# Optimization experiments

Measured on AMD Instinct MI355X. Metric: run time of the kernel, lower is better.

Reference implementation:

```python
import jax, jax.numpy as jnp
import numpy as np

N_NODES = 100000

def _gcn_layer(x, W, b, src, dst, n):
    # x: [N, Fin], W: [Fin, Fout], b: [Fout]; edges src->dst, [E]
    h = x @ W  # [N, Fout]
    # add self loops
    loops = jnp.arange(n, dtype=src.dtype)
    s = jnp.concatenate([src, loops])
    d = jnp.concatenate([dst, loops])
    # symmetric GCN normalization: deg^{-1/2}[s] * deg^{-1/2}[d]
    deg = jax.ops.segment_sum(jnp.ones_like(d, dtype=h.dtype), d, num_segments=n)
    dis = jnp.where(deg > 0, jax.lax.rsqrt(jnp.maximum(deg, 1.0)), 0.0)
    norm = dis[s] * dis[d]  # [E+N]
    msg = h[s] * norm[:, None]  # [E+N, Fout]
    out = jax.ops.segment_sum(msg, d, num_segments=n)  # [N, Fout]
    return out + b


def setup_inputs() -> dict:
    key = jax.random.key(0)
    k1, k2, k3, k4, k5 = jax.random.split(key, 5)
    in_feat, hidden, out_feat = 64, 128, 64
    n_edges = 1600000
    node_features = jax.random.normal(k1, (N_NODES, in_feat), dtype=jnp.float32)
    edge_index = jax.random.randint(k2, (2, n_edges), 0, N_NODES, dtype=jnp.int32)
    # glorot-ish params
    W1 = jax.random.normal(k3, (in_feat, hidden), dtype=jnp.float32) * (1.0 / np.sqrt(in_feat))
    b1 = jnp.zeros((hidden,), dtype=jnp.float32)
    W2 = jax.random.normal(k4, (hidden, out_feat), dtype=jnp.float32) * (1.0 / np.sqrt(hidden))
    b2 = jnp.zeros((out_feat,), dtype=jnp.float32)
    return {"node_features": node_features, "edge_index": edge_index,
            "W1": W1, "b1": b1, "W2": W2, "b2": b2}


def reference(node_features, edge_index, W1, b1, W2, b2):
    src, dst = edge_index[0], edge_index[1]
    n = node_features.shape[0]
    h = _gcn_layer(node_features, W1, b1, src, dst, n)
    h = jax.nn.relu(h)
    h = _gcn_layer(h, W2, b2, src, dst, n)
    return h
```

## Files before the change

kernel.cpp:

```cpp
#include <hip/hip_runtime.h>
#include <hip/hip_fp16.h>

#define NN 100000
#define NB 391
#define NG 512
#define REGION 6144

using f16x8 = __attribute__((ext_vector_type(8))) _Float16;
using f32x4 = __attribute__((ext_vector_type(4))) float;

__global__ __launch_bounds__(256) void bhist_kernel(const int* __restrict__ dst,
                                                    int* __restrict__ counts, int E) {
    __shared__ int h[NB];
    for (int i = threadIdx.x; i < NB; i += 256) h[i] = 0;
    __syncthreads();
    const int g = blockIdx.x;
    const int chunk = (E + NG - 1) / NG;
    const int lo = g * chunk, hi = min(E, lo + chunk);
    for (int e = lo + threadIdx.x; e < hi; e += 256) atomicAdd(&h[dst[e] >> 8], 1);
    __syncthreads();
    for (int i = threadIdx.x; i < NB; i += 256) counts[g * NB + i] = h[i];
}

__global__ __launch_bounds__(256) void bprefix_kernel(int* __restrict__ counts,
                                                      int* __restrict__ btot,
                                                      const float* __restrict__ W1,
                                                      const float* __restrict__ W2,
                                                      __half* __restrict__ W1t,
                                                      __half* __restrict__ W2t) {
    const int b = blockIdx.x, t = threadIdx.x;
    if (b == NB) {
        for (int i = t; i < 64 * 128; i += 256) {
            int k = i / 128, c = i % 128;
            W1t[c * 64 + k] = __float2half(W1[i]);
            int k2 = i / 64, c2 = i % 64;
            W2t[c2 * 128 + k2] = __float2half(W2[i]);
        }
        return;
    }
    __shared__ int sm[256];
    int loc[NG / 256];
    int s = 0;
    #pragma unroll
    for (int p = 0; p < NG / 256; ++p) {
        loc[p] = counts[((NG / 256) * t + p) * NB + b];
        s += loc[p];
    }
    sm[t] = s; __syncthreads();
    for (int off = 1; off < 256; off <<= 1) {
        int x = (t >= off) ? sm[t - off] : 0; __syncthreads();
        sm[t] += x; __syncthreads();
    }
    int run = b * REGION + sm[t] - s;
    #pragma unroll
    for (int p = 0; p < NG / 256; ++p) {
        int c = loc[p];
        counts[((NG / 256) * t + p) * NB + b] = run;
        run += c;
    }
    if (t == 255) btot[b] = sm[255];
}

__global__ __launch_bounds__(256) void bscatter_kernel(const int* __restrict__ src,
                                                       const int* __restrict__ dst,
                                                       const int* __restrict__ cstart,
                                                       int* __restrict__ staging, int E) {
    __shared__ int cur[NB];
    const int g = blockIdx.x;
    for (int i = threadIdx.x; i < NB; i += 256) cur[i] = cstart[g * NB + i];
    __syncthreads();
    const int chunk = (E + NG - 1) / NG;
    const int lo = g * chunk, hi = min(E, lo + chunk);
    for (int e = lo + threadIdx.x; e < hi; e += 256) {
        int d = dst[e];
        int pos = atomicAdd(&cur[d >> 8], 1);
        staging[pos] = src[e] | ((d & 255) << 17);
    }
}

__global__ __launch_bounds__(256) void bfinal_kernel(const int* __restrict__ btot,
                                                     const int* __restrict__ staging,
                                                     int* __restrict__ csr,
                                                     int* __restrict__ row_beg,
                                                     int* __restrict__ row_end,
                                                     float* __restrict__ dis,
                                                     const float* __restrict__ x,
                                                     __half* __restrict__ xh,
                                                     int N) {
    __shared__ int h[256];
    __shared__ int sc[256];
    __shared__ int cur[256];
    __shared__ float sdis[256];
    const int b = blockIdx.x, t = threadIdx.x;
    const int base = b * REGION;
    const int endb = base + btot[b];
    h[t] = 0; __syncthreads();
    for (int i = base + t; i < endb; i += 256) atomicAdd(&h[staging[i] >> 17], 1);
    __syncthreads();
    int v = h[t];
    sc[t] = v; __syncthreads();
    for (int off = 1; off < 256; off <<= 1) {
        int xv = (t >= off) ? sc[t - off] : 0; __syncthreads();
        sc[t] += xv; __syncthreads();
    }
    int excl = sc[t] - v;
    cur[t] = base + excl;
    float dv = rsqrtf((float)v + 1.0f);
    sdis[t] = dv;
    int node = b * 256 + t;
    if (node < N) {
        row_beg[node] = base + excl;
        row_end[node] = base + excl + v;
        dis[node] = dv;
    }
    __syncthreads();
    for (int i = base + t; i < endb; i += 256) {
        int p = staging[i];
        int pos = atomicAdd(&cur[p >> 17], 1);
        csr[pos] = p & 0x1FFFF;
    }
    const int node0 = b * 256;
    const int nmax = min(256, N - node0);
    for (int i = t; i < nmax * 16; i += 256) {
        int nl = i >> 4, c4 = i & 15;
        float4 vx = ((const float4*)x)[(size_t)(node0 + nl) * 16 + c4];
        float wq = sdis[nl];
        __half2* o = (__half2*)&xh[(size_t)(node0 + nl) * 64 + c4 * 4];
        o[0] = __floats2half2_rn(vx.x * wq, vx.y * wq);
        o[1] = __floats2half2_rn(vx.z * wq, vx.w * wq);
    }
}

__global__ __launch_bounds__(512) void gfuse_kernel(const __half* __restrict__ tab,
                                                    const float* __restrict__ dis,
                                                    const __half* __restrict__ W1t,
                                                    const float* __restrict__ b1,
                                                    const __half* __restrict__ W2t,
                                                    const int* __restrict__ row_beg,
                                                    const int* __restrict__ row_end,
                                                    const int* __restrict__ csr,
                                                    __half* __restrict__ zh, int N,
                                                    float one) {
    __shared__ _Float16 sA[16][72];
    __shared__ _Float16 sH[16][136];
    __shared__ float sP[4][16][16];
    const int tid = threadIdx.x;
    const int nodeL = tid >> 5;
    const int l32 = tid & 31;
    const int e = l32 >> 3;
    const int sub = l32 & 7;
    const int node0 = blockIdx.x * 16;
    const int node = node0 + nodeL;
    const int beg = row_beg[node], end = row_end[node];

    float acc[8];
    {
        f16x8 sv = *reinterpret_cast<const f16x8*>(&tab[(size_t)node * 64 + sub * 8]);
        #pragma unroll
        for (int q = 0; q < 8; ++q) acc[q] = (e == 0) ? (float)sv[q] : 0.0f;
    }
    for (int j = beg + e; j < end; j += 4) {
        int s = csr[j];
        f16x8 v = *reinterpret_cast<const f16x8*>(&tab[(size_t)s * 64 + sub * 8]);
        #pragma unroll
        for (int q = 0; q < 8; ++q) acc[q] = fmaf((float)v[q], one, acc[q]);
    }
    #pragma unroll
    for (int q = 0; q < 8; ++q) {
        acc[q] += __shfl_xor(acc[q], 8);
        acc[q] += __shfl_xor(acc[q], 16);
    }
    if (e == 0) {
        const float dd = dis[node];
        f16x8 o;
        #pragma unroll
        for (int q = 0; q < 8; ++q) o[q] = (_Float16)(acc[q] * dd);
        *reinterpret_cast<f16x8*>(&sA[nodeL][sub * 8]) = o;
    }
    __syncthreads();

    const int w = tid >> 6, lane = tid & 63;
    const int lrow = lane & 15, kgrp = lane >> 4;
    {
        const int col = w * 16 + lrow;
        f32x4 a1 = (f32x4){0.f, 0.f, 0.f, 0.f};
        #pragma unroll
        for (int ks = 0; ks < 2; ++ks) {
            const int kbase = ks * 32 + kgrp * 8;
            f16x8 a  = *reinterpret_cast<const f16x8*>(&sA[lrow][kbase]);
            f16x8 bf = *reinterpret_cast<const f16x8*>(&W1t[(size_t)col * 64 + kbase]);
            a1 = __builtin_amdgcn_mfma_f32_16x16x32_f16(a, bf, a1, 0, 0, 0);
        }
        const float bb = b1[col];
        #pragma unroll
        for (int r = 0; r < 4; ++r) {
            const int row = kgrp * 4 + r;
            sH[row][col] = (_Float16)fmaxf(a1[r] + bb, 0.0f);
        }
    }
    __syncthreads();
    {
        const int t2 = w & 3, kh = w >> 2;
        const int col = t2 * 16 + lrow;
        f32x4 a2 = (f32x4){0.f, 0.f, 0.f, 0.f};
        #pragma unroll
        for (int ks = 0; ks < 2; ++ks) {
            const int kbase = kh * 64 + ks * 32 + kgrp * 8;
            f16x8 a  = *reinterpret_cast<const f16x8*>(&sH[lrow][kbase]);
            f16x8 bf = *reinterpret_cast<const f16x8*>(&W2t[(size_t)col * 128 + kbase]);
            a2 = __builtin_amdgcn_mfma_f32_16x16x32_f16(a, bf, a2, 0, 0, 0);
        }
        if (kh == 1) {
            #pragma unroll
            for (int r = 0; r < 4; ++r) sP[t2][kgrp * 4 + r][lrow] = a2[r];
        }
        __syncthreads();
        if (kh == 0) {
            #pragma unroll
            for (int r = 0; r < 4; ++r) {
                const int row = kgrp * 4 + r;
                float v = (a2[r] + sP[t2][row][lrow]) * dis[node0 + row];
                zh[(size_t)(node0 + row) * 64 + col] = __float2half(v);
            }
        }
    }
}

__global__ __launch_bounds__(256) void gather2_kernel(const __half* __restrict__ tab,
                                                      const float* __restrict__ dis,
                                                      const float* __restrict__ b,
                                                      const int* __restrict__ row_beg,
                                                      const int* __restrict__ row_end,
                                                      const int* __restrict__ csr,
                                                      float* __restrict__ out, int N,
                                                      float one) {
    const int node = blockIdx.x * 4 + (threadIdx.x >> 6);
    const int lane = threadIdx.x & 63;
    const int g   = lane >> 3;
    const int sub = lane & 7;
    if (node >= N) return;
    const int beg = row_beg[node], end = row_end[node];

    float acc[8];
    {
        f16x8 sv = *reinterpret_cast<const f16x8*>(&tab[(size_t)node * 64 + sub * 8]);
        #pragma unroll
        for (int q = 0; q < 8; ++q) acc[q] = (g == 0) ? (float)sv[q] : 0.0f;
    }
    int j = beg;
    for (; j + 16 <= end; j += 16) {
        int sA = csr[j + g];
        int sB = csr[j + 8 + g];
        f16x8 vA = *reinterpret_cast<const f16x8*>(&tab[(size_t)sA * 64 + sub * 8]);
        f16x8 vB = *reinterpret_cast<const f16x8*>(&tab[(size_t)sB * 64 + sub * 8]);
        #pragma unroll
        for (int q = 0; q < 8; ++q) acc[q] = fmaf((float)vA[q], one, acc[q]);
        #pragma unroll
        for (int q = 0; q < 8; ++q) acc[q] = fmaf((float)vB[q], one, acc[q]);
    }
    if (j + 8 <= end) {
        int s = csr[j + g];
        f16x8 v = *reinterpret_cast<const f16x8*>(&tab[(size_t)s * 64 + sub * 8]);
        #pragma unroll
        for (int q = 0; q < 8; ++q) acc[q] = fmaf((float)v[q], one, acc[q]);
        j += 8;
    }
    if (j + g < end) {
        int s = csr[j + g];
        f16x8 v = *reinterpret_cast<const f16x8*>(&tab[(size_t)s * 64 + sub * 8]);
        #pragma unroll
        for (int q = 0; q < 8; ++q) acc[q] = fmaf((float)v[q], one, acc[q]);
    }
    #pragma unroll
    for (int q = 0; q < 8; ++q) {
        acc[q] += __shfl_xor(acc[q], 8);
        acc[q] += __shfl_xor(acc[q], 16);
        acc[q] += __shfl_xor(acc[q], 32);
    }
    if (g == 0) {
        const float dd = dis[node];
        float vv[8];
        #pragma unroll
        for (int q = 0; q < 8; ++q) vv[q] = acc[q] * dd + b[sub * 8 + q];
        float* op = &out[(size_t)node * 64 + sub * 8];
        *reinterpret_cast<float4*>(op)     = make_float4(vv[0], vv[1], vv[2], vv[3]);
        *reinterpret_cast<float4*>(op + 4) = make_float4(vv[4], vv[5], vv[6], vv[7]);
    }
}

extern "C" void kernel_launch(void* const* d_in, const int* in_sizes, int n_in,
                              void* d_out, int out_size, void* d_ws, size_t ws_size,
                              hipStream_t stream) {
    const float* x  = (const float*)d_in[0];
    const int*   ei = (const int*)d_in[1];
    const float* W1 = (const float*)d_in[2];
    const float* b1 = (const float*)d_in[3];
    const float* W2 = (const float*)d_in[4];
    const float* b2 = (const float*)d_in[5];
    float* out = (float*)d_out;

    const int N = NN;
    const int E = in_sizes[1] / 2;
    const int* src = ei;
    const int* dst = ei + E;

    int* counts   = (int*)d_ws;
    int* btot     = counts + NG * NB;
    int* row_beg  = btot + 512;
    int* row_end  = row_beg + N;
    float* dis    = (float*)(row_end + N);
    int* staging  = (int*)(dis + N);
    int* csr      = staging + (size_t)NB * REGION;
    float* base   = (float*)(csr + (size_t)NB * REGION);
    __half* xh    = (__half*)base;
    __half* zh    = (__half*)(base + (size_t)N * 32);
    __half* W1t   = (__half*)(base + (size_t)N * 64);
    __half* W2t   = W1t + 128 * 64;

    bhist_kernel<<<NG, 256, 0, stream>>>(dst, counts, E);
    bprefix_kernel<<<NB + 1, 256, 0, stream>>>(counts, btot, W1, W2, W1t, W2t);
    bscatter_kernel<<<NG, 256, 0, stream>>>(src, dst, counts, staging, E);
    bfinal_kernel<<<NB, 256, 0, stream>>>(btot, staging, csr, row_beg, row_end, dis, x, xh, N);

    gfuse_kernel<<<N / 16, 512, 0, stream>>>(xh, dis, W1t, b1, W2t, row_beg, row_end, csr, zh, N, 1.0f);

    gather2_kernel<<<N / 4, 256, 0, stream>>>(zh, dis, b2, row_beg, row_end, csr, out, N, 1.0f);
}
```

Baseline: 166.3 us.

## Split fused gather+GEMM kernel into separate gather and GEMM kernels

Layer-1 aggregation moves out of the fused gather+MFMA kernel into a standalone gather kernel. That kernel uses a full wave per node with 16-wide unrolling and writes an fp16 intermediate, and a separate GEMM kernel then reads it. The aim is to give the gather better occupancy and memory-level parallelism than the 512-thread fused block, where only 4 lanes per feature slice walked each edge list. In exchange it adds an extra kernel launch and a write and read of a 100k×64 fp16 intermediate.

```diff
diff --git a/kernel.cpp b/kernel.cpp
--- a/kernel.cpp
+++ b/kernel.cpp
@@ -131,36 +131,48 @@
     }
 }
 
-__global__ __launch_bounds__(512) void gfuse_kernel(const __half* __restrict__ tab,
-                                                    const float* __restrict__ dis,
-                                                    const __half* __restrict__ W1t,
-                                                    const float* __restrict__ b1,
-                                                    const __half* __restrict__ W2t,
-                                                    const int* __restrict__ row_beg,
-                                                    const int* __restrict__ row_end,
-                                                    const int* __restrict__ csr,
-                                                    __half* __restrict__ zh, int N,
-                                                    float one) {
-    __shared__ _Float16 sA[16][72];
-    __shared__ _Float16 sH[16][136];
-    __shared__ float sP[4][16][16];
-    const int tid = threadIdx.x;
-    const int nodeL = tid >> 5;
-    const int l32 = tid & 31;
-    const int e = l32 >> 3;
-    const int sub = l32 & 7;
-    const int node0 = blockIdx.x * 16;
-    const int node = node0 + nodeL;
+template<bool BIAS, typename OutT>
+__global__ __launch_bounds__(256) void gatherN_kernel(const __half* __restrict__ tab,
+                                                      const float* __restrict__ dis,
+                                                      const float* __restrict__ b,
+                                                      const int* __restrict__ row_beg,
+                                                      const int* __restrict__ row_end,
+                                                      const int* __restrict__ csr,
+                                                      OutT* __restrict__ out, int N,
+                                                      float one) {
+    const int node = blockIdx.x * 4 + (threadIdx.x >> 6);
+    const int lane = threadIdx.x & 63;
+    const int g   = lane >> 3;
+    const int sub = lane & 7;
+    if (node >= N) return;
     const int beg = row_beg[node], end = row_end[node];
 
     float acc[8];
     {
         f16x8 sv = *reinterpret_cast<const f16x8*>(&tab[(size_t)node * 64 + sub * 8]);
         #pragma unroll
-        for (int q = 0; q < 8; ++q) acc[q] = (e == 0) ? (float)sv[q] : 0.0f;
-    }
-    for (int j = beg + e; j < end; j += 4) {
-        int s = csr[j];
+        for (int q = 0; q < 8; ++q) acc[q] = (g == 0) ? (float)sv[q] : 0.0f;
+    }
+    int j = beg;
+    for (; j + 16 <= end; j += 16) {
+        int sA = csr[j + g];
+        int sB = csr[j + 8 + g];
+        f16x8 vA = *reinterpret_cast<const f16x8*>(&tab[(size_t)sA * 64 + sub * 8]);
+        f16x8 vB = *reinterpret_cast<const f16x8*>(&tab[(size_t)sB * 64 + sub * 8]);
+        #pragma unroll
+        for (int q = 0; q < 8; ++q) acc[q] = fmaf((float)vA[q], one, acc[q]);
+        #pragma unroll
+        for (int q = 0; q < 8; ++q) acc[q] = fmaf((float)vB[q], one, acc[q]);
+    }
+    if (j + 8 <= end) {
+        int s = csr[j + g];
+        f16x8 v = *reinterpret_cast<const f16x8*>(&tab[(size_t)s * 64 + sub * 8]);
+        #pragma unroll
+        for (int q = 0; q < 8; ++q) acc[q] = fmaf((float)v[q], one, acc[q]);
+        j += 8;
+    }
+    if (j + g < end) {
+        int s = csr[j + g];
         f16x8 v = *reinterpret_cast<const f16x8*>(&tab[(size_t)s * 64 + sub * 8]);
         #pragma unroll
         for (int q = 0; q < 8; ++q) acc[q] = fmaf((float)v[q], one, acc[q]);
@@ -169,13 +181,45 @@
     for (int q = 0; q < 8; ++q) {
         acc[q] += __shfl_xor(acc[q], 8);
         acc[q] += __shfl_xor(acc[q], 16);
-    }
-    if (e == 0) {
+        acc[q] += __shfl_xor(acc[q], 32);
+    }
+    if (g == 0) {
         const float dd = dis[node];
-        f16x8 o;
-        #pragma unroll
-        for (int q = 0; q < 8; ++q) o[q] = (_Float16)(acc[q] * dd);
-        *reinterpret_cast<f16x8*>(&sA[nodeL][sub * 8]) = o;
+        if constexpr (sizeof(OutT) == 2) {
+            f16x8 o;
+            #pragma unroll
+            for (int q = 0; q < 8; ++q) o[q] = (_Float16)(acc[q] * dd);
+            *reinterpret_cast<f16x8*>(&((__half*)out)[(size_t)node * 64 + sub * 8]) = o;
+        } else {
+            float vv[8];
+            #pragma unroll
+            for (int q = 0; q < 8; ++q) {
+                float v = acc[q] * dd;
+                if (BIAS) v += b[sub * 8 + q];
+                vv[q] = v;
+            }
+            float* op = &((float*)out)[(size_t)node * 64 + sub * 8];
+            *reinterpret_cast<float4*>(op)     = make_float4(vv[0], vv[1], vv[2], vv[3]);
+            *reinterpret_cast<float4*>(op + 4) = make_float4(vv[4], vv[5], vv[6], vv[7]);
+        }
+    }
+}
+
+__global__ __launch_bounds__(512) void gemm12_kernel(const __half* __restrict__ aggh,
+                                                     const float* __restrict__ dis,
+                                                     const __half* __restrict__ W1t,
+                                                     const float* __restrict__ b1,
+                                                     const __half* __restrict__ W2t,
+                                                     __half* __restrict__ zh, int N) {
+    __shared__ _Float16 sA[16][72];
+    __shared__ _Float16 sH[16][132];
+    __shared__ float sP[4][16][16];
+    const int tid = threadIdx.x;
+    const int node0 = blockIdx.x * 16;
+    if (tid < 128) {
+        int r = tid >> 3, c8 = tid & 7;
+        *reinterpret_cast<f16x8*>(&sA[r][c8 * 8]) =
+            *reinterpret_cast<const f16x8*>(&aggh[(size_t)(node0 + r) * 64 + c8 * 8]);
     }
     __syncthreads();
 
@@ -223,68 +267,6 @@
                 zh[(size_t)(node0 + row) * 64 + col] = __float2half(v);
             }
         }
-    }
-}
-
-__global__ __launch_bounds__(256) void gather2_kernel(const __half* __restrict__ tab,
-                                                      const float* __restrict__ dis,
-                                                      const float* __restrict__ b,
-                                                      const int* __restrict__ row_beg,
-                                                      const int* __restrict__ row_end,
-                                                      const int* __restrict__ csr,
-                                                      float* __restrict__ out, int N,
-                                                      float one) {
-    const int node = blockIdx.x * 4 + (threadIdx.x >> 6);
-    const int lane = threadIdx.x & 63;
-    const int g   = lane >> 3;
-    const int sub = lane & 7;
-    if (node >= N) return;
-    const int beg = row_beg[node], end = row_end[node];
-
-    float acc[8];
-    {
-        f16x8 sv = *reinterpret_cast<const f16x8*>(&tab[(size_t)node * 64 + sub * 8]);
-        #pragma unroll
-        for (int q = 0; q < 8; ++q) acc[q] = (g == 0) ? (float)sv[q] : 0.0f;
-    }
-    int j = beg;
-    for (; j + 16 <= end; j += 16) {
-        int sA = csr[j + g];
-        int sB = csr[j + 8 + g];
-        f16x8 vA = *reinterpret_cast<const f16x8*>(&tab[(size_t)sA * 64 + sub * 8]);
-        f16x8 vB = *reinterpret_cast<const f16x8*>(&tab[(size_t)sB * 64 + sub * 8]);
-        #pragma unroll
-        for (int q = 0; q < 8; ++q) acc[q] = fmaf((float)vA[q], one, acc[q]);
-        #pragma unroll
-        for (int q = 0; q < 8; ++q) acc[q] = fmaf((float)vB[q], one, acc[q]);
-    }
-    if (j + 8 <= end) {
-        int s = csr[j + g];
-        f16x8 v = *reinterpret_cast<const f16x8*>(&tab[(size_t)s * 64 + sub * 8]);
-        #pragma unroll
-        for (int q = 0; q < 8; ++q) acc[q] = fmaf((float)v[q], one, acc[q]);
-        j += 8;
-    }
-    if (j + g < end) {
-        int s = csr[j + g];
-        f16x8 v = *reinterpret_cast<const f16x8*>(&tab[(size_t)s * 64 + sub * 8]);
-        #pragma unroll
-        for (int q = 0; q < 8; ++q) acc[q] = fmaf((float)v[q], one, acc[q]);
-    }
-    #pragma unroll
-    for (int q = 0; q < 8; ++q) {
-        acc[q] += __shfl_xor(acc[q], 8);
-        acc[q] += __shfl_xor(acc[q], 16);
-        acc[q] += __shfl_xor(acc[q], 32);
-    }
-    if (g == 0) {
-        const float dd = dis[node];
-        float vv[8];
-        #pragma unroll
-        for (int q = 0; q < 8; ++q) vv[q] = acc[q] * dd + b[sub * 8 + q];
-        float* op = &out[(size_t)node * 64 + sub * 8];
-        *reinterpret_cast<float4*>(op)     = make_float4(vv[0], vv[1], vv[2], vv[3]);
-        *reinterpret_cast<float4*>(op + 4) = make_float4(vv[4], vv[5], vv[6], vv[7]);
     }
 }
 
@@ -305,7 +287,7 @@
     const int* dst = ei + E;
 
     int* counts   = (int*)d_ws;
-    int* btot     = counts + NG * NB;
+    int* btot     = counts + (size_t)NG * NB;
     int* row_beg  = btot + 512;
     int* row_end  = row_beg + N;
     float* dis    = (float*)(row_end + N);
@@ -313,8 +295,9 @@
     int* csr      = staging + (size_t)NB * REGION;
     float* base   = (float*)(csr + (size_t)NB * REGION);
     __half* xh    = (__half*)base;
-    __half* zh    = (__half*)(base + (size_t)N * 32);
-    __half* W1t   = (__half*)(base + (size_t)N * 64);
+    __half* aggh  = (__half*)(base + (size_t)N * 32);
+    __half* zh    = (__half*)(base + (size_t)N * 64);
+    __half* W1t   = (__half*)(base + (size_t)N * 96);
     __half* W2t   = W1t + 128 * 64;
 
     bhist_kernel<<<NG, 256, 0, stream>>>(dst, counts, E);
@@ -322,7 +305,8 @@
     bscatter_kernel<<<NG, 256, 0, stream>>>(src, dst, counts, staging, E);
     bfinal_kernel<<<NB, 256, 0, stream>>>(btot, staging, csr, row_beg, row_end, dis, x, xh, N);
 
-    gfuse_kernel<<<N / 16, 512, 0, stream>>>(xh, dis, W1t, b1, W2t, row_beg, row_end, csr, zh, N, 1.0f);
-
-    gather2_kernel<<<N / 4, 256, 0, stream>>>(zh, dis, b2, row_beg, row_end, csr, out, N, 1.0f);
-}
+    gatherN_kernel<false, __half><<<N / 4, 256, 0, stream>>>(xh, dis, nullptr, row_beg, row_end, csr, aggh, N, 1.0f);
+    gemm12_kernel<<<N / 16, 512, 0, stream>>>(aggh, dis, W1t, b1, W2t, zh, N);
+
+    gatherN_kernel<true, float><<<N / 4, 256, 0, stream>>>(zh, dis, b2, row_beg, row_end, csr, out, N, 1.0f);
+}
```

Result: slower. 174.5 us (+4.9%).
